# Performance work log

Measured on AMD Instinct MI355X. Metric: run time of the kernel, lower is better.

## Reference

```python
import jax, jax.numpy as jnp
import numpy as np

N = 50000      # nodes
E = 800000     # edges (before self loops)
IN = 128       # in_channels
H = 8          # heads
C = 32         # hidden_channels per head
HC = H * C     # 256, concat head dim
G = 256        # number of graphs
NEG_SLOPE = 0.2  # PyG GATConv default


def gat_conv(h_in, src, dst, W, att_s, att_d, bias):
    """PyG-style GATConv, concat heads. src/dst include self loops.
    h_in: [N, F_in]; W: [H*C, F_in]; att_s/att_d: [H, C]; bias: [H*C]."""
    h = (h_in @ W.T).reshape(N, H, C)                      # [N,H,C]
    a_s = jnp.sum(h * att_s, axis=-1)                      # [N,H]
    a_d = jnp.sum(h * att_d, axis=-1)                      # [N,H]
    e = jax.nn.leaky_relu(a_s[src] + a_d[dst], NEG_SLOPE)  # [E',H]
    # segment softmax over incoming edges of each dst node
    m = jax.ops.segment_max(e, dst, num_segments=N)        # [N,H]
    p = jnp.exp(e - m[dst])                                # [E',H]
    denom = jax.ops.segment_sum(p, dst, num_segments=N)    # [N,H]
    alpha = p / denom[dst]                                 # [E',H]
    msg = alpha[:, :, None] * h[src]                       # [E',H,C]
    out = jax.ops.segment_sum(msg, dst, num_segments=N)    # [N,H,C]
    return out.reshape(N, HC) + bias


def setup_inputs() -> dict:
    key = jax.random.key(0)
    ks = jax.random.split(key, 20)
    s = 0.1
    inp = {
        "x": jax.random.normal(ks[0], (N, IN), jnp.float32),
        "edge_index": jax.random.randint(ks[1], (2, E), 0, N, dtype=jnp.int64),
        "batch": jnp.sort(jax.random.randint(ks[2], (N,), 0, G, dtype=jnp.int64)),
        # layer 1: IN -> H*C
        "W1": jax.random.normal(ks[3], (HC, IN), jnp.float32) * s,
        "as1": jax.random.normal(ks[4], (H, C), jnp.float32) * s,
        "ad1": jax.random.normal(ks[5], (H, C), jnp.float32) * s,
        "b1": jnp.zeros((HC,), jnp.float32),
        # layer 2: H*C -> H*C
        "W2": jax.random.normal(ks[6], (HC, HC), jnp.float32) * s,
        "as2": jax.random.normal(ks[7], (H, C), jnp.float32) * s,
        "ad2": jax.random.normal(ks[8], (H, C), jnp.float32) * s,
        "b2": jnp.zeros((HC,), jnp.float32),
        # layer 3: H*C -> H*C
        "W3": jax.random.normal(ks[9], (HC, HC), jnp.float32) * s,
        "as3": jax.random.normal(ks[10], (H, C), jnp.float32) * s,
        "ad3": jax.random.normal(ks[11], (H, C), jnp.float32) * s,
        "b3": jnp.zeros((HC,), jnp.float32),
        # final linear H*C -> 1
        "Wf": jax.random.normal(ks[12], (1, HC), jnp.float32) * s,
        "bf": jnp.zeros((1,), jnp.float32),
    }
    return inp


def reference(x, edge_index, batch, W1, as1, ad1, b1, W2, as2, ad2, b2,
              W3, as3, ad3, b3, Wf, bf):
    # add self loops once (PyG GATConv default add_self_loops=True)
    loop = jnp.arange(N, dtype=edge_index.dtype)
    src = jnp.concatenate([edge_index[0], loop])
    dst = jnp.concatenate([edge_index[1], loop])

    h = jax.nn.relu(gat_conv(x, src, dst, W1, as1, ad1, b1))
    # dropout p=0.01, eval mode -> identity
    h = jax.nn.relu(gat_conv(h, src, dst, W2, as2, ad2, b2))
    h = gat_conv(h, src, dst, W3, as3, ad3, b3)

    # global mean pool per graph
    sums = jax.ops.segment_sum(h, batch, num_segments=G)          # [G,HC]
    cnt = jax.ops.segment_sum(jnp.ones((N, 1), h.dtype), batch, num_segments=G)
    pooled = sums / jnp.maximum(cnt, 1.0)                         # [G,HC]
    return pooled @ Wf.T + bf                                     # [G,1]
```

## Files before the change

kernel.cpp:

```cpp
#include <hip/hip_runtime.h>

#define N_NODES 50000
#define E_EDGES 800000
#define E_EXT   850000
#define IN_CH   128
#define HC      256
#define NHEAD   8
#define CH      32
#define NGRAPH  256
#define SCAN_CHUNK 1024
#define N_CHUNKS ((N_NODES + SCAN_CHUNK - 1) / SCAN_CHUNK)

typedef __bf16 bf16x8 __attribute__((ext_vector_type(8)));
typedef float  f32x4  __attribute__((ext_vector_type(4)));

__device__ inline ushort f2bf(float f) {
    union { float f; unsigned u; } v; v.f = f;
    unsigned u = v.u;
    unsigned r = u + 0x7FFFu + ((u >> 16) & 1u);
    return (ushort)(r >> 16);
}
__device__ inline float bflo(unsigned u) {
    union { unsigned u; float f; } v; v.u = u << 16; return v.f;
}
__device__ inline float bfhi(unsigned u) {
    union { unsigned u; float f; } v; v.u = u & 0xFFFF0000u; return v.f;
}

#define W1_N4 (HC * IN_CH / 4)
#define W23_N4 (HC * HC / 4)
__global__ __launch_bounds__(256) void cvt_weights_kernel(
    const float* __restrict__ W1, const float* __restrict__ W2,
    const float* __restrict__ W3,
    ushort* __restrict__ W1b, ushort* __restrict__ W2b, ushort* __restrict__ W3b)
{
    int i = blockIdx.x * blockDim.x + threadIdx.x;
    const float* src; ushort* dst; int k;
    if (i < W1_N4) { src = W1; dst = W1b; k = i; }
    else if (i < W1_N4 + W23_N4) { src = W2; dst = W2b; k = i - W1_N4; }
    else if (i < W1_N4 + 2 * W23_N4) { src = W3; dst = W3b; k = i - W1_N4 - W23_N4; }
    else return;
    float4 v = *(const float4*)(src + (size_t)k * 4);
    ushort4 o;
    o.x = f2bf(v.x); o.y = f2bf(v.y); o.z = f2bf(v.z); o.w = f2bf(v.w);
    *(ushort4*)(dst + (size_t)k * 4) = o;
}

__global__ void bw_kernel(const float* __restrict__ b3, const float* __restrict__ Wf,
                          float* __restrict__ bw)
{
    int h = threadIdx.x;
    if (h >= NHEAD) return;
    float s = 0.f;
    for (int c = 0; c < CH; c++) s += b3[h * CH + c] * Wf[h * CH + c];
    bw[h] = s;
}

__global__ __launch_bounds__(256) void mfma_gemm_kernel(
    const ushort* __restrict__ Xb, const float* __restrict__ Xf,
    const ushort* __restrict__ Wb,
    ushort* __restrict__ Hb, int M, int F,
    const float* __restrict__ att_s, const float* __restrict__ att_d,
    const float* __restrict__ wf,
    float* __restrict__ as_out, float* __restrict__ ad_out,
    float2* __restrict__ q_out)
{
    __shared__ ushort As[128][40];
    __shared__ ushort Bs[128][40];
    const int tid  = threadIdx.x;
    const int lane = tid & 63;
    const int wave = tid >> 6;
    const int wr = (wave >> 1) * 64;
    const int wc = (wave & 1) * 64;
    const int bm = blockIdx.x * 128;
    const int bn = blockIdx.y * 128;
    const int lrow = tid >> 2;
    const int lseg = (tid & 3) * 8;
    const int fr = lane & 15;
    const int fk = (lane >> 4) * 8;

    f32x4 zero = {0.f, 0.f, 0.f, 0.f};
    f32x4 acc[4][4];
    #pragma unroll
    for (int i = 0; i < 4; i++)
        #pragma unroll
        for (int j = 0; j < 4; j++) acc[i][j] = zero;

    for (int k0 = 0; k0 < F; k0 += 32) {
        #pragma unroll
        for (int rr = 0; rr < 2; rr++) {
            int row = lrow + rr * 64;
            int arow = bm + row;
            bf16x8 av = {};
            if (Xf) {
                if (arow < M) {
                    float4 lo = *(const float4*)(Xf + (size_t)arow * F + k0 + lseg);
                    float4 hi = *(const float4*)(Xf + (size_t)arow * F + k0 + lseg + 4);
                    ushort t[8] = { f2bf(lo.x), f2bf(lo.y), f2bf(lo.z), f2bf(lo.w),
                                    f2bf(hi.x), f2bf(hi.y), f2bf(hi.z), f2bf(hi.w) };
                    av = *(const bf16x8*)t;
                }
            } else {
                if (arow < M) av = *(const bf16x8*)(Xb + (size_t)arow * F + k0 + lseg);
            }
            *(bf16x8*)(&As[row][lseg]) = av;
            bf16x8 bv = *(const bf16x8*)(Wb + (size_t)(bn + row) * F + k0 + lseg);
            *(bf16x8*)(&Bs[row][lseg]) = bv;
        }
        __syncthreads();
        bf16x8 a[4], b[4];
        #pragma unroll
        for (int i = 0; i < 4; i++) {
            a[i] = *(const bf16x8*)(&As[wr + i * 16 + fr][fk]);
            b[i] = *(const bf16x8*)(&Bs[wc + i * 16 + fr][fk]);
        }
        #pragma unroll
        for (int i = 0; i < 4; i++)
            #pragma unroll
            for (int j = 0; j < 4; j++)
                acc[i][j] = __builtin_amdgcn_mfma_f32_16x16x32_bf16(
                    a[i], b[j], acc[i][j], 0, 0, 0);
        __syncthreads();
    }

    const int rb = (lane >> 4) * 4;
    const int h0 = (bn >> 5) + (wc >> 5);

    const float wsa0 = att_s[h0 * CH + fr],        wsa1 = att_s[h0 * CH + 16 + fr];
    const float wda0 = att_d[h0 * CH + fr],        wda1 = att_d[h0 * CH + 16 + fr];
    const float wsb0 = att_s[(h0 + 1) * CH + fr],  wsb1 = att_s[(h0 + 1) * CH + 16 + fr];
    const float wdb0 = att_d[(h0 + 1) * CH + fr],  wdb1 = att_d[(h0 + 1) * CH + 16 + fr];
    float wfa0 = 0.f, wfa1 = 0.f, wfb0 = 0.f, wfb1 = 0.f;
    if (wf) {
        wfa0 = wf[h0 * CH + fr];       wfa1 = wf[h0 * CH + 16 + fr];
        wfb0 = wf[(h0 + 1) * CH + fr]; wfb1 = wf[(h0 + 1) * CH + 16 + fr];
    }

    #pragma unroll
    for (int i = 0; i < 4; i++) {
        #pragma unroll
        for (int r = 0; r < 4; r++) {
            int m = bm + wr + i * 16 + rb + r;
            if (Hb && m < M) {
                #pragma unroll
                for (int j = 0; j < 4; j++)
                    Hb[(size_t)m * HC + bn + wc + j * 16 + fr] = f2bf(acc[i][j][r]);
            }
            float psa = acc[i][0][r] * wsa0 + acc[i][1][r] * wsa1;
            float pda = acc[i][0][r] * wda0 + acc[i][1][r] * wda1;
            float psb = acc[i][2][r] * wsb0 + acc[i][3][r] * wsb1;
            float pdb = acc[i][2][r] * wdb0 + acc[i][3][r] * wdb1;
            float pwa = 0.f, pwb = 0.f;
            if (wf) {
                pwa = acc[i][0][r] * wfa0 + acc[i][1][r] * wfa1;
                pwb = acc[i][2][r] * wfb0 + acc[i][3][r] * wfb1;
            }
            #pragma unroll
            for (int off = 1; off < 16; off <<= 1) {
                psa += __shfl_xor(psa, off);
                pda += __shfl_xor(pda, off);
                psb += __shfl_xor(psb, off);
                pdb += __shfl_xor(pdb, off);
                if (wf) { pwa += __shfl_xor(pwa, off); pwb += __shfl_xor(pwb, off); }
            }
            if (fr == 0 && m < M) {
                if (q_out) {
                    q_out[m * NHEAD + h0]     = make_float2(psa, pwa);
                    q_out[m * NHEAD + h0 + 1] = make_float2(psb, pwb);
                } else {
                    as_out[m * NHEAD + h0]     = psa;
                    as_out[m * NHEAD + h0 + 1] = psb;
                }
                ad_out[m * NHEAD + h0]     = pda;
                ad_out[m * NHEAD + h0 + 1] = pdb;
            }
        }
    }
}

__global__ __launch_bounds__(256) void hist_kernel(
    const int* __restrict__ ei, int* __restrict__ deg)
{
    int eid = blockIdx.x * blockDim.x + threadIdx.x;
    if (eid >= E_EXT) return;
    int d = (eid < E_EDGES) ? ei[E_EDGES + eid] : (eid - E_EDGES);
    atomicAdd(&deg[d], 1);
}

__global__ void scan1_kernel(const int* __restrict__ deg,
                             int* __restrict__ row_ptr, int* __restrict__ csum)
{
    __shared__ int buf[SCAN_CHUNK];
    int t = threadIdx.x;
    int base = blockIdx.x * SCAN_CHUNK;
    int v = (base + t < N_NODES) ? deg[base + t] : 0;
    buf[t] = v;
    __syncthreads();
    for (int off = 1; off < SCAN_CHUNK; off <<= 1) {
        int x = buf[t];
        int y = (t >= off) ? buf[t - off] : 0;
        __syncthreads();
        buf[t] = x + y;
        __syncthreads();
    }
    if (base + t < N_NODES) row_ptr[base + t] = buf[t] - v;
    if (t == SCAN_CHUNK - 1) csum[blockIdx.x] = buf[t];
}

__global__ void scan2_kernel(int* __restrict__ csum)
{
    __shared__ int buf[64];
    int t = threadIdx.x;
    int v = (t < N_CHUNKS) ? csum[t] : 0;
    buf[t] = v;
    __syncthreads();
    for (int off = 1; off < 64; off <<= 1) {
        int x = buf[t];
        int y = (t >= off) ? buf[t - off] : 0;
        __syncthreads();
        buf[t] = x + y;
        __syncthreads();
    }
    if (t < N_CHUNKS) csum[t] = buf[t] - v;
}

__global__ void scan3_kernel(int* __restrict__ row_ptr, const int* __restrict__ csum)
{
    int i = blockIdx.x * blockDim.x + threadIdx.x;
    if (i < N_NODES) row_ptr[i] += csum[i / SCAN_CHUNK];
    if (i == 0) row_ptr[N_NODES] = E_EXT;
}

__global__ __launch_bounds__(256) void scatter_kernel(
    const int* __restrict__ ei, const int* __restrict__ row_ptr,
    int* __restrict__ cur, int* __restrict__ esrc)
{
    int eid = blockIdx.x * blockDim.x + threadIdx.x;
    if (eid >= E_EXT) return;
    int s, d;
    if (eid < E_EDGES) { s = ei[eid]; d = ei[E_EDGES + eid]; }
    else { s = eid - E_EDGES; d = s; }
    int pos = row_ptr[d] + atomicAdd(&cur[d], 1);
    esrc[pos] = s;
}

__global__ __launch_bounds__(256) void gather_kernel(
    const int* __restrict__ row_ptr, const int* __restrict__ esrc,
    const ushort* __restrict__ hb,
    const float* __restrict__ a_s, const float* __restrict__ a_d,
    const float* __restrict__ bias,
    ushort* __restrict__ out_b)
{
    int wv = (blockIdx.x * blockDim.x + threadIdx.x) >> 6;
    int lane = threadIdx.x & 63;
    int half = lane >> 5;
    int lloc = lane & 31;
    int n = wv * 2 + half;
    if (n >= N_NODES) return;
    const int hh = lloc >> 2;
    const int shbase = half << 5;
    const float adv = a_d[n * NHEAD + hh];
    const int beg = row_ptr[n], end = row_ptr[n + 1];

    float a0=0.f,a1=0.f,a2=0.f,a3=0.f,a4=0.f,a5=0.f,a6=0.f,a7=0.f,den=0.f;

    for (int base = beg; base < end; base += 32) {
        int cnt = min(32, end - base);
        int sv = (base + lloc < end) ? esrc[base + lloc] : 0;
        int j = 0;
        for (; j + 4 <= cnt; j += 4) {
            int s0 = __shfl(sv, shbase + j);
            int s1 = __shfl(sv, shbase + j + 1);
            int s2 = __shfl(sv, shbase + j + 2);
            int s3 = __shfl(sv, shbase + j + 3);
            float e0 = a_s[s0 * NHEAD + hh];
            float e1 = a_s[s1 * NHEAD + hh];
            float e2 = a_s[s2 * NHEAD + hh];
            float e3 = a_s[s3 * NHEAD + hh];
            uint4 u0 = *(const uint4*)(hb + (size_t)s0 * HC + lloc * 8);
            uint4 u1 = *(const uint4*)(hb + (size_t)s1 * HC + lloc * 8);
            uint4 u2 = *(const uint4*)(hb + (size_t)s2 * HC + lloc * 8);
            uint4 u3 = *(const uint4*)(hb + (size_t)s3 * HC + lloc * 8);
            e0 += adv; e0 = (e0 > 0.f) ? e0 : 0.2f * e0; float w0 = __expf(e0);
            e1 += adv; e1 = (e1 > 0.f) ? e1 : 0.2f * e1; float w1 = __expf(e1);
            e2 += adv; e2 = (e2 > 0.f) ? e2 : 0.2f * e2; float w2 = __expf(e2);
            e3 += adv; e3 = (e3 > 0.f) ? e3 : 0.2f * e3; float w3 = __expf(e3);
            den += (w0 + w1) + (w2 + w3);
            a0 = fmaf(w0, bflo(u0.x), a0); a1 = fmaf(w0, bfhi(u0.x), a1);
            a2 = fmaf(w0, bflo(u0.y), a2); a3 = fmaf(w0, bfhi(u0.y), a3);
            a4 = fmaf(w0, bflo(u0.z), a4); a5 = fmaf(w0, bfhi(u0.z), a5);
            a6 = fmaf(w0, bflo(u0.w), a6); a7 = fmaf(w0, bfhi(u0.w), a7);
            a0 = fmaf(w1, bflo(u1.x), a0); a1 = fmaf(w1, bfhi(u1.x), a1);
            a2 = fmaf(w1, bflo(u1.y), a2); a3 = fmaf(w1, bfhi(u1.y), a3);
            a4 = fmaf(w1, bflo(u1.z), a4); a5 = fmaf(w1, bfhi(u1.z), a5);
            a6 = fmaf(w1, bflo(u1.w), a6); a7 = fmaf(w1, bfhi(u1.w), a7);
            a0 = fmaf(w2, bflo(u2.x), a0); a1 = fmaf(w2, bfhi(u2.x), a1);
            a2 = fmaf(w2, bflo(u2.y), a2); a3 = fmaf(w2, bfhi(u2.y), a3);
            a4 = fmaf(w2, bflo(u2.z), a4); a5 = fmaf(w2, bfhi(u2.z), a5);
            a6 = fmaf(w2, bflo(u2.w), a6); a7 = fmaf(w2, bfhi(u2.w), a7);
            a0 = fmaf(w3, bflo(u3.x), a0); a1 = fmaf(w3, bfhi(u3.x), a1);
            a2 = fmaf(w3, bflo(u3.y), a2); a3 = fmaf(w3, bfhi(u3.y), a3);
            a4 = fmaf(w3, bflo(u3.z), a4); a5 = fmaf(w3, bfhi(u3.z), a5);
            a6 = fmaf(w3, bflo(u3.w), a6); a7 = fmaf(w3, bfhi(u3.w), a7);
        }
        for (; j < cnt; j++) {
            int s = __shfl(sv, shbase + j);
            float e = a_s[s * NHEAD + hh] + adv;
            e = (e > 0.f) ? e : 0.2f * e;
            float w = __expf(e);
            den += w;
            uint4 u = *(const uint4*)(hb + (size_t)s * HC + lloc * 8);
            a0 = fmaf(w, bflo(u.x), a0); a1 = fmaf(w, bfhi(u.x), a1);
            a2 = fmaf(w, bflo(u.y), a2); a3 = fmaf(w, bfhi(u.y), a3);
            a4 = fmaf(w, bflo(u.z), a4); a5 = fmaf(w, bfhi(u.z), a5);
            a6 = fmaf(w, bflo(u.w), a6); a7 = fmaf(w, bfhi(u.w), a7);
        }
    }
    float inv = 1.f / den;
    float4 ba = *(const float4*)(bias + lloc * 8);
    float4 bb = *(const float4*)(bias + lloc * 8 + 4);
    float o0 = fmaf(a0, inv, ba.x), o1 = fmaf(a1, inv, ba.y);
    float o2 = fmaf(a2, inv, ba.z), o3 = fmaf(a3, inv, ba.w);
    float o4 = fmaf(a4, inv, bb.x), o5 = fmaf(a5, inv, bb.y);
    float o6 = fmaf(a6, inv, bb.z), o7 = fmaf(a7, inv, bb.w);
    o0 = fmaxf(o0, 0.f); o1 = fmaxf(o1, 0.f); o2 = fmaxf(o2, 0.f); o3 = fmaxf(o3, 0.f);
    o4 = fmaxf(o4, 0.f); o5 = fmaxf(o5, 0.f); o6 = fmaxf(o6, 0.f); o7 = fmaxf(o7, 0.f);
    uint4 ob;
    ob.x = (unsigned)f2bf(o0) | ((unsigned)f2bf(o1) << 16);
    ob.y = (unsigned)f2bf(o2) | ((unsigned)f2bf(o3) << 16);
    ob.z = (unsigned)f2bf(o4) | ((unsigned)f2bf(o5) << 16);
    ob.w = (unsigned)f2bf(o6) | ((unsigned)f2bf(o7) << 16);
    *(uint4*)(out_b + (size_t)n * HC + lloc * 8) = ob;
}

__global__ __launch_bounds__(256) void light_gather_kernel(
    const int* __restrict__ row_ptr, const int* __restrict__ esrc,
    const float2* __restrict__ q, const float* __restrict__ a_d,
    const float* __restrict__ bw, float* __restrict__ ndot)
{
    int idx = blockIdx.x * blockDim.x + threadIdx.x;
    if (idx >= N_NODES * NHEAD) return;
    int n = idx >> 3, hh = idx & 7;
    const float adv = a_d[idx];
    const int beg = row_ptr[n], end = row_ptr[n + 1];
    float acc = 0.f, den = 0.f;
    int e = beg;
    for (; e + 4 <= end; e += 4) {
        int s0 = esrc[e], s1 = esrc[e + 1], s2 = esrc[e + 2], s3 = esrc[e + 3];
        float2 q0 = q[s0 * NHEAD + hh];
        float2 q1 = q[s1 * NHEAD + hh];
        float2 q2 = q[s2 * NHEAD + hh];
        float2 q3 = q[s3 * NHEAD + hh];
        float t0 = q0.x + adv; t0 = (t0 > 0.f) ? t0 : 0.2f * t0; float w0 = __expf(t0);
        float t1 = q1.x + adv; t1 = (t1 > 0.f) ? t1 : 0.2f * t1; float w1 = __expf(t1);
        float t2 = q2.x + adv; t2 = (t2 > 0.f) ? t2 : 0.2f * t2; float w2 = __expf(t2);
        float t3 = q3.x + adv; t3 = (t3 > 0.f) ? t3 : 0.2f * t3; float w3 = __expf(t3);
        den += (w0 + w1) + (w2 + w3);
        acc = fmaf(w0, q0.y, acc); acc = fmaf(w1, q1.y, acc);
        acc = fmaf(w2, q2.y, acc); acc = fmaf(w3, q3.y, acc);
    }
    for (; e < end; e++) {
        int s = esrc[e];
        float2 qv = q[s * NHEAD + hh];
        float t = qv.x + adv; t = (t > 0.f) ? t : 0.2f * t;
        float w = __expf(t);
        den += w;
        acc = fmaf(w, qv.y, acc);
    }
    float p = acc / den + bw[hh];
    #pragma unroll
    for (int off = 4; off > 0; off >>= 1) p += __shfl_xor(p, off);
    if (hh == 0) ndot[n] = p;
}

__global__ __launch_bounds__(256) void pool2_kernel(
    const float* __restrict__ ndot, const int* __restrict__ batch,
    const float* __restrict__ bf, float* __restrict__ outp)
{
    __shared__ float red[256];
    int g = blockIdx.x, t = threadIdx.x;
    int lo = 0, hi = N_NODES;
    while (lo < hi) { int mid = (lo + hi) >> 1; if (batch[mid] < g) lo = mid + 1; else hi = mid; }
    int start = lo;
    lo = 0; hi = N_NODES;
    while (lo < hi) { int mid = (lo + hi) >> 1; if (batch[mid] < g + 1) lo = mid + 1; else hi = mid; }
    int end = lo;
    float s = 0.f;
    for (int i = start + t; i < end; i += 256) s += ndot[i];
    red[t] = s;
    __syncthreads();
    for (int k = 128; k > 0; k >>= 1) {
        if (t < k) red[t] += red[t + k];
        __syncthreads();
    }
    if (t == 0) outp[g] = red[0] / fmaxf((float)(end - start), 1.f) + bf[0];
}

extern "C" void kernel_launch(void* const* d_in, const int* in_sizes, int n_in,
                              void* d_out, int out_size, void* d_ws, size_t ws_size,
                              hipStream_t stream)
{
    const float* x    = (const float*)d_in[0];
    const int*   ei   = (const int*)d_in[1];
    const int*   batch= (const int*)d_in[2];
    const float* W1   = (const float*)d_in[3];
    const float* as1  = (const float*)d_in[4];
    const float* ad1  = (const float*)d_in[5];
    const float* b1   = (const float*)d_in[6];
    const float* W2   = (const float*)d_in[7];
    const float* as2  = (const float*)d_in[8];
    const float* ad2  = (const float*)d_in[9];
    const float* b2   = (const float*)d_in[10];
    const float* W3   = (const float*)d_in[11];
    const float* as3  = (const float*)d_in[12];
    const float* ad3  = (const float*)d_in[13];
    const float* b3   = (const float*)d_in[14];
    const float* Wf   = (const float*)d_in[15];
    const float* bf   = (const float*)d_in[16];
    float* out = (float*)d_out;

    char* ws = (char*)d_ws;
    size_t off = 0;
    auto allocb = [&](size_t bytes) {
        void* p = ws + off;
        off += (bytes + 255) & ~(size_t)255;
        return p;
    };
    ushort* bufA    = (ushort*)allocb((size_t)N_NODES * HC * 2);
    ushort* bufB    = (ushort*)allocb((size_t)N_NODES * HC * 2);
    ushort* W1b     = (ushort*)allocb((size_t)HC * IN_CH * 2);
    ushort* W2b     = (ushort*)allocb((size_t)HC * HC * 2);
    ushort* W3b     = (ushort*)allocb((size_t)HC * HC * 2);
    float*  as_buf  = (float*) allocb((size_t)N_NODES * NHEAD * 4);
    float*  ad_buf  = (float*) allocb((size_t)N_NODES * NHEAD * 4);
    float2* q_buf   = (float2*)allocb((size_t)N_NODES * NHEAD * 8);
    float*  bw_buf  = (float*) allocb(NHEAD * 4);
    int*    deg     = (int*)   allocb(N_NODES * 4);
    int*    cur     = (int*)   allocb(N_NODES * 4);
    int*    row_ptr = (int*)   allocb((N_NODES + 1) * 4);
    int*    csum    = (int*)   allocb(64 * 4);
    int*    esrc    = (int*)   allocb(E_EXT * 4);
    float*  ndot    = (float*) allocb(N_NODES * 4);
    (void)ws_size; (void)in_sizes; (void)n_in; (void)out_size;

    cvt_weights_kernel<<<(W1_N4 + 2 * W23_N4 + 255) / 256, 256, 0, stream>>>(
        W1, W2, W3, W1b, W2b, W3b);
    bw_kernel<<<1, 64, 0, stream>>>(b3, Wf, bw_buf);

    hipMemsetAsync(deg, 0, N_NODES * sizeof(int), stream);
    hipMemsetAsync(cur, 0, N_NODES * sizeof(int), stream);
    hist_kernel<<<(E_EXT + 255) / 256, 256, 0, stream>>>(ei, deg);
    scan1_kernel<<<N_CHUNKS, SCAN_CHUNK, 0, stream>>>(deg, row_ptr, csum);
    scan2_kernel<<<1, 64, 0, stream>>>(csum);
    scan3_kernel<<<(N_NODES + 255) / 256, 256, 0, stream>>>(row_ptr, csum);
    scatter_kernel<<<(E_EXT + 255) / 256, 256, 0, stream>>>(ei, row_ptr, cur, esrc);

    dim3 ggrid((N_NODES + 127) / 128, HC / 128);
    const int gather_blocks = (((N_NODES + 1) / 2) * 64 + 255) / 256;

    mfma_gemm_kernel<<<ggrid, 256, 0, stream>>>(
        nullptr, x, W1b, bufB, N_NODES, IN_CH, as1, ad1, nullptr,
        as_buf, ad_buf, nullptr);
    gather_kernel<<<gather_blocks, 256, 0, stream>>>(
        row_ptr, esrc, bufB, as_buf, ad_buf, b1, bufA);
    mfma_gemm_kernel<<<ggrid, 256, 0, stream>>>(
        bufA, nullptr, W2b, bufB, N_NODES, HC, as2, ad2, nullptr,
        as_buf, ad_buf, nullptr);
    gather_kernel<<<gather_blocks, 256, 0, stream>>>(
        row_ptr, esrc, bufB, as_buf, ad_buf, b2, bufA);
    mfma_gemm_kernel<<<ggrid, 256, 0, stream>>>(
        bufA, nullptr, W3b, nullptr, N_NODES, HC, as3, ad3, Wf,
        nullptr, ad_buf, q_buf);
    light_gather_kernel<<<(N_NODES * NHEAD + 255) / 256, 256, 0, stream>>>(
        row_ptr, esrc, q_buf, ad_buf, bw_buf, ndot);

    pool2_kernel<<<NGRAPH, 256, 0, stream>>>(ndot, batch, bf, out);
}
```

Measured before the change: 358.8 us.

## Fold attention and final-linear vectors into W3 to shrink layer-3 GEMM

Layer 3's full features are never stored, only per-head projections against att_s, att_d and Wf. The change precomputes a 32x256 matrix V whose rows are those vectors multiplied through W3, so layer 3 becomes a thin GEMM with 24 useful outputs instead of 256. It also folds the bias-dot kernel into the weight-conversion kernel and merges the two memsets into one. This trades a small amount of extra setup work and bf16 rounding of the folded weights for a much smaller layer-3 matmul.

```diff
diff --git a/kernel.cpp b/kernel.cpp
--- a/kernel.cpp
+++ b/kernel.cpp
@@ -29,31 +29,45 @@
 
 #define W1_N4 (HC * IN_CH / 4)
 #define W23_N4 (HC * HC / 4)
+#define CVT_N4 (W1_N4 + 2 * W23_N4)
+#define COMP_N (32 * HC)
 __global__ __launch_bounds__(256) void cvt_weights_kernel(
     const float* __restrict__ W1, const float* __restrict__ W2,
     const float* __restrict__ W3,
-    ushort* __restrict__ W1b, ushort* __restrict__ W2b, ushort* __restrict__ W3b)
+    ushort* __restrict__ W1b, ushort* __restrict__ W2b, ushort* __restrict__ W3b,
+    const float* __restrict__ as3, const float* __restrict__ ad3,
+    const float* __restrict__ b3, const float* __restrict__ Wf,
+    float* __restrict__ bw, ushort* __restrict__ Vb)
 {
     int i = blockIdx.x * blockDim.x + threadIdx.x;
-    const float* src; ushort* dst; int k;
-    if (i < W1_N4) { src = W1; dst = W1b; k = i; }
-    else if (i < W1_N4 + W23_N4) { src = W2; dst = W2b; k = i - W1_N4; }
-    else if (i < W1_N4 + 2 * W23_N4) { src = W3; dst = W3b; k = i - W1_N4 - W23_N4; }
-    else return;
-    float4 v = *(const float4*)(src + (size_t)k * 4);
-    ushort4 o;
-    o.x = f2bf(v.x); o.y = f2bf(v.y); o.z = f2bf(v.z); o.w = f2bf(v.w);
-    *(ushort4*)(dst + (size_t)k * 4) = o;
-}
-
-__global__ void bw_kernel(const float* __restrict__ b3, const float* __restrict__ Wf,
-                          float* __restrict__ bw)
-{
-    int h = threadIdx.x;
-    if (h >= NHEAD) return;
-    float s = 0.f;
-    for (int c = 0; c < CH; c++) s += b3[h * CH + c] * Wf[h * CH + c];
-    bw[h] = s;
+    if (blockIdx.x == 0 && threadIdx.x < NHEAD) {
+        float s = 0.f;
+        for (int c = 0; c < CH; c++)
+            s += b3[threadIdx.x * CH + c] * Wf[threadIdx.x * CH + c];
+        bw[threadIdx.x] = s;
+    }
+    if (i < CVT_N4) {
+        const float* src; ushort* dst; int k;
+        if (i < W1_N4) { src = W1; dst = W1b; k = i; }
+        else if (i < W1_N4 + W23_N4) { src = W2; dst = W2b; k = i - W1_N4; }
+        else { src = W3; dst = W3b; k = i - W1_N4 - W23_N4; }
+        float4 v = *(const float4*)(src + (size_t)k * 4);
+        ushort4 o;
+        o.x = f2bf(v.x); o.y = f2bf(v.y); o.z = f2bf(v.z); o.w = f2bf(v.w);
+        *(ushort4*)(dst + (size_t)k * 4) = o;
+        return;
+    }
+    int c2 = i - CVT_N4;
+    if (c2 >= COMP_N) return;
+    int j = c2 >> 8, k = c2 & 255;
+    float v = 0.f;
+    if (j < 24) {
+        int h = j & 7;
+        const float* aw = (j < 8) ? as3 : (j < 16 ? Wf : ad3);
+        for (int c = 0; c < CH; c++)
+            v += aw[h * CH + c] * W3[(size_t)(h * CH + c) * HC + k];
+    }
+    Vb[j * HC + k] = f2bf(v);
 }
 
 __global__ __launch_bounds__(256) void mfma_gemm_kernel(
@@ -61,9 +75,7 @@
     const ushort* __restrict__ Wb,
     ushort* __restrict__ Hb, int M, int F,
     const float* __restrict__ att_s, const float* __restrict__ att_d,
-    const float* __restrict__ wf,
-    float* __restrict__ as_out, float* __restrict__ ad_out,
-    float2* __restrict__ q_out)
+    float* __restrict__ as_out, float* __restrict__ ad_out)
 {
     __shared__ ushort As[128][40];
     __shared__ ushort Bs[128][40];
@@ -130,18 +142,13 @@
     const float wda0 = att_d[h0 * CH + fr],        wda1 = att_d[h0 * CH + 16 + fr];
     const float wsb0 = att_s[(h0 + 1) * CH + fr],  wsb1 = att_s[(h0 + 1) * CH + 16 + fr];
     const float wdb0 = att_d[(h0 + 1) * CH + fr],  wdb1 = att_d[(h0 + 1) * CH + 16 + fr];
-    float wfa0 = 0.f, wfa1 = 0.f, wfb0 = 0.f, wfb1 = 0.f;
-    if (wf) {
-        wfa0 = wf[h0 * CH + fr];       wfa1 = wf[h0 * CH + 16 + fr];
-        wfb0 = wf[(h0 + 1) * CH + fr]; wfb1 = wf[(h0 + 1) * CH + 16 + fr];
-    }
 
     #pragma unroll
     for (int i = 0; i < 4; i++) {
         #pragma unroll
         for (int r = 0; r < 4; r++) {
             int m = bm + wr + i * 16 + rb + r;
-            if (Hb && m < M) {
+            if (m < M) {
                 #pragma unroll
                 for (int j = 0; j < 4; j++)
                     Hb[(size_t)m * HC + bn + wc + j * 16 + fr] = f2bf(acc[i][j][r]);
@@ -150,29 +157,89 @@
             float pda = acc[i][0][r] * wda0 + acc[i][1][r] * wda1;
             float psb = acc[i][2][r] * wsb0 + acc[i][3][r] * wsb1;
             float pdb = acc[i][2][r] * wdb0 + acc[i][3][r] * wdb1;
-            float pwa = 0.f, pwb = 0.f;
-            if (wf) {
-                pwa = acc[i][0][r] * wfa0 + acc[i][1][r] * wfa1;
-                pwb = acc[i][2][r] * wfb0 + acc[i][3][r] * wfb1;
-            }
             #pragma unroll
             for (int off = 1; off < 16; off <<= 1) {
                 psa += __shfl_xor(psa, off);
                 pda += __shfl_xor(pda, off);
                 psb += __shfl_xor(psb, off);
                 pdb += __shfl_xor(pdb, off);
-                if (wf) { pwa += __shfl_xor(pwa, off); pwb += __shfl_xor(pwb, off); }
             }
             if (fr == 0 && m < M) {
-                if (q_out) {
-                    q_out[m * NHEAD + h0]     = make_float2(psa, pwa);
-                    q_out[m * NHEAD + h0 + 1] = make_float2(psb, pwb);
-                } else {
-                    as_out[m * NHEAD + h0]     = psa;
-                    as_out[m * NHEAD + h0 + 1] = psb;
-                }
+                as_out[m * NHEAD + h0]     = psa;
+                as_out[m * NHEAD + h0 + 1] = psb;
                 ad_out[m * NHEAD + h0]     = pda;
                 ad_out[m * NHEAD + h0 + 1] = pdb;
+            }
+        }
+    }
+}
+
+__global__ __launch_bounds__(256) void gemm3_kernel(
+    const ushort* __restrict__ Xb, const ushort* __restrict__ Vb, int M,
+    float2* __restrict__ q_out, float* __restrict__ ad_out)
+{
+    __shared__ ushort As[128][40];
+    __shared__ ushort Bs[32][40];
+    const int tid  = threadIdx.x;
+    const int lane = tid & 63;
+    const int wave = tid >> 6;
+    const int bm = blockIdx.x * 128;
+    const int lrow = tid >> 2;
+    const int lseg = (tid & 3) * 8;
+    const int fr = lane & 15;
+    const int fk = (lane >> 4) * 8;
+
+    f32x4 zero = {0.f, 0.f, 0.f, 0.f};
+    f32x4 acc[2][2];
+    #pragma unroll
+    for (int i = 0; i < 2; i++)
+        #pragma unroll
+        for (int j = 0; j < 2; j++) acc[i][j] = zero;
+
+    for (int k0 = 0; k0 < HC; k0 += 32) {
+        #pragma unroll
+        for (int rr = 0; rr < 2; rr++) {
+            int row = lrow + rr * 64;
+            int arow = bm + row;
+            bf16x8 av = {};
+            if (arow < M) av = *(const bf16x8*)(Xb + (size_t)arow * HC + k0 + lseg);
+            *(bf16x8*)(&As[row][lseg]) = av;
+        }
+        if (tid < 128) {
+            int brow = tid >> 2;
+            bf16x8 bv = *(const bf16x8*)(Vb + (size_t)brow * HC + k0 + lseg);
+            *(bf16x8*)(&Bs[brow][lseg]) = bv;
+        }
+        __syncthreads();
+        bf16x8 a[2], b[2];
+        #pragma unroll
+        for (int i = 0; i < 2; i++) {
+            a[i] = *(const bf16x8*)(&As[wave * 32 + i * 16 + fr][fk]);
+            b[i] = *(const bf16x8*)(&Bs[i * 16 + fr][fk]);
+        }
+        #pragma unroll
+        for (int i = 0; i < 2; i++)
+            #pragma unroll
+            for (int j = 0; j < 2; j++)
+                acc[i][j] = __builtin_amdgcn_mfma_f32_16x16x32_bf16(
+                    a[i], b[j], acc[i][j], 0, 0, 0);
+        __syncthreads();
+    }
+
+    const int rb = (lane >> 4) * 4;
+    #pragma unroll
+    for (int i = 0; i < 2; i++) {
+        #pragma unroll
+        for (int r = 0; r < 4; r++) {
+            int m = bm + wave * 32 + i * 16 + rb + r;
+            if (m >= M) continue;
+            #pragma unroll
+            for (int j = 0; j < 2; j++) {
+                int jj = j * 16 + fr;
+                float v = acc[i][j][r];
+                if (jj < 8)       ((float*)q_out)[(size_t)(m * NHEAD + jj) * 2]     = v;
+                else if (jj < 16) ((float*)q_out)[(size_t)(m * NHEAD + jj - 8) * 2 + 1] = v;
+                else if (jj < 24) ad_out[m * NHEAD + jj - 16] = v;
             }
         }
     }
@@ -431,6 +498,7 @@
     ushort* W1b     = (ushort*)allocb((size_t)HC * IN_CH * 2);
     ushort* W2b     = (ushort*)allocb((size_t)HC * HC * 2);
     ushort* W3b     = (ushort*)allocb((size_t)HC * HC * 2);
+    ushort* Vb      = (ushort*)allocb((size_t)32 * HC * 2);
     float*  as_buf  = (float*) allocb((size_t)N_NODES * NHEAD * 4);
     float*  ad_buf  = (float*) allocb((size_t)N_NODES * NHEAD * 4);
     float2* q_buf   = (float2*)allocb((size_t)N_NODES * NHEAD * 8);
@@ -443,12 +511,11 @@
     float*  ndot    = (float*) allocb(N_NODES * 4);
     (void)ws_size; (void)in_sizes; (void)n_in; (void)out_size;
 
-    cvt_weights_kernel<<<(W1_N4 + 2 * W23_N4 + 255) / 256, 256, 0, stream>>>(
-        W1, W2, W3, W1b, W2b, W3b);
-    bw_kernel<<<1, 64, 0, stream>>>(b3, Wf, bw_buf);
-
-    hipMemsetAsync(deg, 0, N_NODES * sizeof(int), stream);
-    hipMemsetAsync(cur, 0, N_NODES * sizeof(int), stream);
+    cvt_weights_kernel<<<(CVT_N4 + COMP_N + 255) / 256, 256, 0, stream>>>(
+        W1, W2, W3, W1b, W2b, W3b, as3, ad3, b3, Wf, bw_buf, Vb);
+
+    const size_t deg_pad = ((size_t)N_NODES * 4 + 255) & ~(size_t)255;
+    hipMemsetAsync(deg, 0, deg_pad + (size_t)N_NODES * 4, stream);
     hist_kernel<<<(E_EXT + 255) / 256, 256, 0, stream>>>(ei, deg);
     scan1_kernel<<<N_CHUNKS, SCAN_CHUNK, 0, stream>>>(deg, row_ptr, csum);
     scan2_kernel<<<1, 64, 0, stream>>>(csum);
@@ -459,18 +526,15 @@
     const int gather_blocks = (((N_NODES + 1) / 2) * 64 + 255) / 256;
 
     mfma_gemm_kernel<<<ggrid, 256, 0, stream>>>(
-        nullptr, x, W1b, bufB, N_NODES, IN_CH, as1, ad1, nullptr,
-        as_buf, ad_buf, nullptr);
+        nullptr, x, W1b, bufB, N_NODES, IN_CH, as1, ad1, as_buf, ad_buf);
     gather_kernel<<<gather_blocks, 256, 0, stream>>>(
         row_ptr, esrc, bufB, as_buf, ad_buf, b1, bufA);
     mfma_gemm_kernel<<<ggrid, 256, 0, stream>>>(
-        bufA, nullptr, W2b, bufB, N_NODES, HC, as2, ad2, nullptr,
-        as_buf, ad_buf, nullptr);
+        bufA, nullptr, W2b, bufB, N_NODES, HC, as2, ad2, as_buf, ad_buf);
     gather_kernel<<<gather_blocks, 256, 0, stream>>>(
         row_ptr, esrc, bufB, as_buf, ad_buf, b2, bufA);
-    mfma_gemm_kernel<<<ggrid, 256, 0, stream>>>(
-        bufA, nullptr, W3b, nullptr, N_NODES, HC, as3, ad3, Wf,
-        nullptr, ad_buf, q_buf);
+    gemm3_kernel<<<(N_NODES + 127) / 128, 256, 0, stream>>>(
+        bufA, Vb, N_NODES, q_buf, ad_buf);
     light_gather_kernel<<<(N_NODES * NHEAD + 255) / 256, 256, 0, stream>>>(
         row_ptr, esrc, q_buf, ad_buf, bw_buf, ndot);
 
```

Measured after the change: 319.1 us. -11.1%, faster.
